# Kernel optimization log

Hardware: AMD Instinct MI355X
Metric: run time of the kernel (lower is better)

Reference implementation:

```python
import jax, jax.numpy as jnp
import numpy as np

K = 5              # kernel_size per pseudo dim
K3 = K ** 3        # 125 kernel weight slots
BITS = np.array([[(c >> d) & 1 for d in range(3)] for c in range(8)], dtype=np.int32)  # [8,3]
STRIDES = np.array([1, K, K * K], dtype=np.int32)

N0, E0 = 16384, 262144
N1, E1 = 4096, 65536
N2, E2 = 1024, 16384
N3, E3 = 256, 4096
B = 16
V = B * 8          # final dense 2x2x2 voxels per graph


def spline_conv(x, src, dst, pseudo, W, root, bias, num_nodes):
    """Degree-1 open B-spline conv (torch SplineConv, mean aggr + root + bias).
    x: [N,in], pseudo: [E,3] in [0,1], W: [K^3,in,out]."""
    v = pseudo * (K - 1)                         # [E,3]
    lo = jnp.clip(jnp.floor(v), 0, K - 2)
    frac = v - lo                                # [E,3]
    lo = lo.astype(jnp.int32)
    bits = jnp.asarray(BITS)                     # [8,3]
    idx = lo[:, None, :] + bits[None]            # [E,8,3]
    kidx = (idx * jnp.asarray(STRIDES)).sum(-1)  # [E,8] flat kernel index
    basis = jnp.where(bits[None].astype(bool), frac[:, None, :], 1.0 - frac[:, None, :]).prod(-1)  # [E,8]
    y = jnp.einsum('ni,kio->nko', x, W)          # [N,K3,out] per-node per-kernel transform
    yv = y[src[:, None], kidx]                   # [E,8,out] gather
    msg = (basis[..., None] * yv).sum(1)         # [E,out]
    agg = jax.ops.segment_sum(msg, dst, num_segments=num_nodes)
    deg = jax.ops.segment_sum(jnp.ones(dst.shape[0], x.dtype), dst, num_segments=num_nodes)
    agg = agg / jnp.maximum(deg, 1.0)[:, None]   # mean aggregation
    return agg + x @ root + bias


def pool_max(x, cluster, num_segments):
    p = jax.ops.segment_max(x, cluster, num_segments=num_segments)
    return jnp.where(jnp.isfinite(p), p, 0.0)    # empty voxels -> 0


def setup_inputs() -> dict:
    key = jax.random.key(0)
    ks = iter(jax.random.split(key, 64))
    f = lambda s, sc: jax.random.normal(next(ks), s, jnp.float32) * sc
    u = lambda s: jax.random.uniform(next(ks), s, jnp.float32)
    ri = lambda s, hi: jax.random.randint(next(ks), s, 0, hi, dtype=jnp.int32)
    return dict(
        x0=u((N0, 1)),
        pseudo0=u((E0, 3)), pseudo1=u((E1, 3)), pseudo2=u((E2, 3)), pseudo3=u((E3, 3)),
        W1=f((K3, 1, 32), 0.3), root1=f((1, 32), 0.3), b1=f((32,), 0.05),
        W2=f((K3, 32, 64), 0.05), root2=f((32, 64), 0.05), b2=f((64,), 0.05),
        W3=f((K3, 64, 64), 0.04), root3=f((64, 64), 0.04), b3=f((64,), 0.05),
        W4=f((K3, 64, 128), 0.04), root4=f((64, 128), 0.04), b4=f((128,), 0.05),
        fc1_w=f((1024, 256), 0.03), fc1_b=f((256,), 0.05),
        fc2_w=f((256, 10), 0.06), fc2_b=f((10,), 0.05),
        src0=ri((E0,), N0), dst0=ri((E0,), N0),
        src1=ri((E1,), N1), dst1=ri((E1,), N1),
        src2=ri((E2,), N2), dst2=ri((E2,), N2),
        src3=ri((E3,), N3), dst3=ri((E3,), N3),
        cluster0=ri((N0,), N1), cluster1=ri((N1,), N2),
        cluster2=ri((N2,), N3), cluster3=ri((N3,), V),
    )


def reference(x0, pseudo0, pseudo1, pseudo2, pseudo3,
              W1, root1, b1, W2, root2, b2, W3, root3, b3, W4, root4, b4,
              fc1_w, fc1_b, fc2_w, fc2_b,
              src0, dst0, src1, dst1, src2, dst2, src3, dst3,
              cluster0, cluster1, cluster2, cluster3):
    x = jax.nn.elu(spline_conv(x0, src0, dst0, pseudo0, W1, root1, b1, N0))
    x = pool_max(x, cluster0, N1)
    x = jax.nn.elu(spline_conv(x, src1, dst1, pseudo1, W2, root2, b2, N1))
    x = pool_max(x, cluster1, N2)
    x = jax.nn.elu(spline_conv(x, src2, dst2, pseudo2, W3, root3, b3, N2))
    x = pool_max(x, cluster2, N3)
    x = jax.nn.elu(spline_conv(x, src3, dst3, pseudo3, W4, root4, b4, N3))
    x = pool_max(x, cluster3, V)                 # [B*8, 128]
    x = x.reshape(B, 8 * 128)
    x = jax.nn.elu(x @ fc1_w + fc1_b)
    x = x @ fc2_w + fc2_b                        # dropout is a no-op in eval
    return jax.nn.log_softmax(x, axis=1)
```

## Files before the change

### kernel.cpp

```cpp
#include <hip/hip_runtime.h>
#include <hip/hip_bf16.h>
#include <math.h>

namespace {

constexpr int KK = 5;
constexpr int K3 = 125;
constexpr int N0 = 16384, E0 = 262144;
constexpr int N1 = 4096,  E1 = 65536;
constexpr int N2 = 1024,  E2 = 16384;
constexpr int N3 = 256,   E3 = 4096;
constexpr int NV = 128;
constexpr int BB = 16;

constexpr size_t OFF_AGG1 = 0;
constexpr size_t OFF_AGG2 = OFF_AGG1 + (size_t)N0 * 32;
constexpr size_t OFF_AGG3 = OFF_AGG2 + (size_t)N1 * 64;
constexpr size_t OFF_AGG4 = OFF_AGG3 + (size_t)N2 * 64;
constexpr size_t OFF_DEG1 = OFF_AGG4 + (size_t)N3 * 128;
constexpr size_t OFF_DEG2 = OFF_DEG1 + N0;
constexpr size_t OFF_DEG3 = OFF_DEG2 + N1;
constexpr size_t OFF_DEG4 = OFF_DEG3 + N2;
constexpr size_t ZERO_END = OFF_DEG4 + N3;

constexpr size_t OFF_PENC1 = ZERO_END;
constexpr size_t OFF_PENC2 = OFF_PENC1 + (size_t)N1 * 32;
constexpr size_t OFF_PENC3 = OFF_PENC2 + (size_t)N2 * 64;
constexpr size_t OFF_PENC4 = OFF_PENC3 + (size_t)N3 * 64;
constexpr size_t PENC_END  = OFF_PENC4 + (size_t)NV * 128;
constexpr size_t PENC_TOTAL = PENC_END - ZERO_END;

constexpr size_t OFF_X1 = PENC_END;
constexpr size_t OFF_P1 = OFF_X1 + (size_t)N0 * 32;
constexpr size_t OFF_X2 = OFF_P1 + (size_t)N1 * 32;
constexpr size_t OFF_P2 = OFF_X2 + (size_t)N1 * 64;
constexpr size_t OFF_X3 = OFF_P2 + (size_t)N2 * 64;
constexpr size_t OFF_P3 = OFF_X3 + (size_t)N2 * 64;
constexpr size_t OFF_X4 = OFF_P3 + (size_t)N3 * 64;
constexpr size_t OFF_P4 = OFF_X4 + (size_t)N3 * 128;
constexpr size_t OFF_FC1 = OFF_P4 + (size_t)NV * 128;
constexpr size_t WS_FLOATS = OFF_FC1 + (size_t)BB * 256;

constexpr size_t OFF_Y = WS_FLOATS;
constexpr size_t Y_ELEMS_MAX = (size_t)N1 * K3 * 64;
constexpr size_t WS_NEED_BYTES = OFF_Y * 4 + Y_ELEMS_MAX * 2;

__device__ __forceinline__ float eluf(float x) { return x > 0.f ? x : expm1f(x); }

__device__ __forceinline__ unsigned enc_f(float x) {
    unsigned u = __float_as_uint(x);
    return (u & 0x80000000u) ? ~u : (u | 0x80000000u);
}
__device__ __forceinline__ float dec_f(unsigned u) {
    u = (u & 0x80000000u) ? (u & 0x7fffffffu) : ~u;
    return __uint_as_float(u);
}

__device__ __forceinline__ void decode_edge(const float* __restrict__ pseudo, int e,
                                            float bas[8], int kid[8]) {
    float v0 = pseudo[e * 3 + 0] * (KK - 1);
    float v1 = pseudo[e * 3 + 1] * (KK - 1);
    float v2 = pseudo[e * 3 + 2] * (KK - 1);
    float f0 = fminf(fmaxf(floorf(v0), 0.f), (float)(KK - 2));
    float f1 = fminf(fmaxf(floorf(v1), 0.f), (float)(KK - 2));
    float f2 = fminf(fmaxf(floorf(v2), 0.f), (float)(KK - 2));
    int lo0 = (int)f0, lo1 = (int)f1, lo2 = (int)f2;
    float fr0 = v0 - f0, fr1 = v1 - f1, fr2 = v2 - f2;
#pragma unroll
    for (int c = 0; c < 8; ++c) {
        int b0 = c & 1, b1 = (c >> 1) & 1, b2 = (c >> 2) & 1;
        kid[c] = (lo0 + b0) + (lo1 + b1) * KK + (lo2 + b2) * KK * KK;
        bas[c] = (b0 ? fr0 : 1.f - fr0) * (b1 ? fr1 : 1.f - fr1) * (b2 ? fr2 : 1.f - fr2);
    }
}

__global__ void init_enc(unsigned* __restrict__ p, int n) {
    int g = blockIdx.x * blockDim.x + threadIdx.x;
    if (g < n) p[g] = 0x007FFFFFu;
}

__global__ void spline_l1(const float* __restrict__ x,
                          const float* __restrict__ pseudo,
                          const float* __restrict__ W1,
                          const int* __restrict__ src,
                          const int* __restrict__ dst,
                          float* __restrict__ agg,
                          float* __restrict__ deg, int E) {
    __shared__ float wlds[K3 * 32];
    int tid = threadIdx.x;
    for (int i = tid; i < K3 * 32; i += 256) wlds[i] = W1[i];
    __syncthreads();
    int o = tid & 31;
    int esub = tid >> 5;
    int ebase = blockIdx.x * 32 + esub;
#pragma unroll
    for (int r = 0; r < 4; ++r) {
        int e = ebase + r * 8;
        if (e >= E) continue;
        float bas[8]; int kid[8];
        decode_edge(pseudo, e, bas, kid);
        int s = src[e], dn = dst[e];
        float xv = x[s];
        float acc = 0.f;
#pragma unroll
        for (int c = 0; c < 8; ++c)
            acc = fmaf(bas[c], wlds[kid[c] * 32 + o], acc);
        atomicAdd(&agg[(size_t)dn * 32 + o], xv * acc);
        if (o == 0) atomicAdd(&deg[dn], 1.f);
    }
}

template <int IN, int OUT>
__global__ void gemm_y(const float* __restrict__ x,
                       const float* __restrict__ W,
                       __hip_bfloat16* __restrict__ y, int N) {
    constexpr int KO = K3 * OUT;
    __shared__ float xs[32][IN];
    int kt = blockIdx.x % (KO / 64);
    int n0 = (blockIdx.x / (KO / 64)) * 32;
    int tid = threadIdx.x;
    for (int idx = tid; idx < 32 * IN; idx += 256)
        xs[idx / IN][idx % IN] = x[(size_t)(n0 + idx / IN) * IN + idx % IN];
    __syncthreads();
    int col = kt * 64 + (tid & 63);
    int nsub = tid >> 6;
    int k = col / OUT, o = col % OUT;
    const float* Wp = W + (size_t)k * IN * OUT + o;
    float acc[8] = {0.f, 0.f, 0.f, 0.f, 0.f, 0.f, 0.f, 0.f};
#pragma unroll 4
    for (int i = 0; i < IN; ++i) {
        float w = Wp[(size_t)i * OUT];
#pragma unroll
        for (int j = 0; j < 8; ++j)
            acc[j] = fmaf(xs[nsub * 8 + j][i], w, acc[j]);
    }
#pragma unroll
    for (int j = 0; j < 8; ++j)
        y[(size_t)(n0 + nsub * 8 + j) * KO + col] = __float2bfloat16(acc[j]);
}

template <int OUT>
__global__ void gather_edge(const __hip_bfloat16* __restrict__ y,
                            const float* __restrict__ pseudo,
                            const int* __restrict__ src,
                            const int* __restrict__ dst,
                            float* __restrict__ agg,
                            float* __restrict__ deg, int E) {
    long long g = (long long)blockIdx.x * blockDim.x + threadIdx.x;
    int e = (int)(g / OUT);
    int o = (int)(g % OUT);
    if (e >= E) return;
    float bas[8]; int kid[8];
    decode_edge(pseudo, e, bas, kid);
    int s = src[e], dn = dst[e];
    const __hip_bfloat16* yp = y + (size_t)s * (K3 * OUT) + o;
    float acc = 0.f;
#pragma unroll
    for (int c = 0; c < 8; ++c)
        acc = fmaf(bas[c], __bfloat162float(yp[(size_t)kid[c] * OUT]), acc);
    atomicAdd(&agg[(size_t)dn * OUT + o], acc);
    if (o == 0) atomicAdd(&deg[dn], 1.f);
}

template <int IN, int OUT>
__global__ void spline_edge(const float* __restrict__ x,
                            const float* __restrict__ pseudo,
                            const float* __restrict__ W,
                            const int* __restrict__ src,
                            const int* __restrict__ dst,
                            float* __restrict__ agg,
                            float* __restrict__ deg, int E) {
    long long g = (long long)blockIdx.x * blockDim.x + threadIdx.x;
    int e = (int)(g / OUT);
    int o = (int)(g % OUT);
    if (e >= E) return;
    float bas[8]; int kid[8];
    decode_edge(pseudo, e, bas, kid);
    int s = src[e], dn = dst[e];
    const float* xp = x + (size_t)s * IN;
    float acc = 0.f;
#pragma unroll
    for (int c = 0; c < 8; ++c) {
        const float* Wp = W + (size_t)kid[c] * IN * OUT + o;
        float sacc = 0.f;
        for (int i = 0; i < IN; ++i)
            sacc = fmaf(xp[i], Wp[(size_t)i * OUT], sacc);
        acc = fmaf(bas[c], sacc, acc);
    }
    atomicAdd(&agg[(size_t)dn * OUT + o], acc);
    if (o == 0) atomicAdd(&deg[dn], 1.f);
}

template <int IN, int OUT>
__global__ void node_finish(const float* __restrict__ agg,
                            const float* __restrict__ deg,
                            const float* __restrict__ x,
                            const float* __restrict__ root,
                            const float* __restrict__ bias,
                            float* __restrict__ out, int N) {
    int g = blockIdx.x * blockDim.x + threadIdx.x;
    if (g >= N * OUT) return;
    int n = g / OUT, o = g % OUT;
    float r = 0.f;
    for (int i = 0; i < IN; ++i)
        r = fmaf(x[(size_t)n * IN + i], root[(size_t)i * OUT + o], r);
    float dg = fmaxf(deg[n], 1.f);
    float val = agg[g] / dg + r + bias[o];
    out[g] = eluf(val);
}

template <int C>
__global__ void pool_scatter(const float* __restrict__ x,
                             const int* __restrict__ cluster,
                             unsigned* __restrict__ penc, int N) {
    int g = blockIdx.x * blockDim.x + threadIdx.x;
    if (g >= N * C) return;
    int n = g / C, c = g % C;
    atomicMax(&penc[(size_t)cluster[n] * C + c], enc_f(x[g]));
}

__global__ void pool_final(const unsigned* __restrict__ penc,
                           float* __restrict__ out, int M) {
    int g = blockIdx.x * blockDim.x + threadIdx.x;
    if (g >= M) return;
    float v = dec_f(penc[g]);
    out[g] = isfinite(v) ? v : 0.f;
}

__global__ void fc1_kernel(const float* __restrict__ xin,
                           const float* __restrict__ w,
                           const float* __restrict__ b,
                           float* __restrict__ out) {
    int bq = blockIdx.x;
    int p = threadIdx.x;
    const float* xr = xin + (size_t)bq * 1024;
    float acc = b[p];
    for (int q = 0; q < 1024; ++q)
        acc = fmaf(xr[q], w[(size_t)q * 256 + p], acc);
    out[(size_t)bq * 256 + p] = eluf(acc);
}

__global__ void fc2_ls_kernel(const float* __restrict__ xin,
                              const float* __restrict__ w,
                              const float* __restrict__ b,
                              float* __restrict__ out) {
    __shared__ float l[10];
    __shared__ float red[2];
    int bq = blockIdx.x;
    int t = threadIdx.x;
    if (t < 10) {
        const float* xr = xin + (size_t)bq * 256;
        float acc = b[t];
        for (int q = 0; q < 256; ++q)
            acc = fmaf(xr[q], w[(size_t)q * 10 + t], acc);
        l[t] = acc;
    }
    __syncthreads();
    if (t == 0) {
        float m = l[0];
        for (int i = 1; i < 10; ++i) m = fmaxf(m, l[i]);
        float s = 0.f;
        for (int i = 0; i < 10; ++i) s += expf(l[i] - m);
        red[0] = m;
        red[1] = logf(s);
    }
    __syncthreads();
    if (t < 10) out[(size_t)bq * 10 + t] = l[t] - red[0] - red[1];
}

inline unsigned blk(long long t) { return (unsigned)((t + 255) / 256); }

}

extern "C" void kernel_launch(void* const* d_in, const int* in_sizes, int n_in,
                              void* d_out, int out_size, void* d_ws, size_t ws_size,
                              hipStream_t stream) {
    const float* x0    = (const float*)d_in[0];
    const float* ps0   = (const float*)d_in[1];
    const float* ps1   = (const float*)d_in[2];
    const float* ps2   = (const float*)d_in[3];
    const float* ps3   = (const float*)d_in[4];
    const float* W1    = (const float*)d_in[5];
    const float* root1 = (const float*)d_in[6];
    const float* b1    = (const float*)d_in[7];
    const float* W2    = (const float*)d_in[8];
    const float* root2 = (const float*)d_in[9];
    const float* b2    = (const float*)d_in[10];
    const float* W3    = (const float*)d_in[11];
    const float* root3 = (const float*)d_in[12];
    const float* b3    = (const float*)d_in[13];
    const float* W4    = (const float*)d_in[14];
    const float* root4 = (const float*)d_in[15];
    const float* b4    = (const float*)d_in[16];
    const float* fc1w  = (const float*)d_in[17];
    const float* fc1b  = (const float*)d_in[18];
    const float* fc2w  = (const float*)d_in[19];
    const float* fc2b  = (const float*)d_in[20];
    const int* src0 = (const int*)d_in[21];
    const int* dst0 = (const int*)d_in[22];
    const int* src1 = (const int*)d_in[23];
    const int* dst1 = (const int*)d_in[24];
    const int* src2 = (const int*)d_in[25];
    const int* dst2 = (const int*)d_in[26];
    const int* src3 = (const int*)d_in[27];
    const int* dst3 = (const int*)d_in[28];
    const int* cl0  = (const int*)d_in[29];
    const int* cl1  = (const int*)d_in[30];
    const int* cl2  = (const int*)d_in[31];
    const int* cl3  = (const int*)d_in[32];

    float* ws = (float*)d_ws;
    float* out = (float*)d_out;
    __hip_bfloat16* yb = (__hip_bfloat16*)(ws + OFF_Y);
    const bool use_y = (ws_size >= WS_NEED_BYTES);

    hipMemsetAsync(ws + OFF_AGG1, 0, ZERO_END * sizeof(float), stream);
    init_enc<<<blk(PENC_TOTAL), 256, 0, stream>>>((unsigned*)(ws + OFF_PENC1), (int)PENC_TOTAL);

    spline_l1<<<E0 / 32, 256, 0, stream>>>(x0, ps0, W1, src0, dst0,
                                           ws + OFF_AGG1, ws + OFF_DEG1, E0);
    node_finish<1, 32><<<blk((long long)N0 * 32), 256, 0, stream>>>(
        ws + OFF_AGG1, ws + OFF_DEG1, x0, root1, b1, ws + OFF_X1, N0);
    pool_scatter<32><<<blk((long long)N0 * 32), 256, 0, stream>>>(
        ws + OFF_X1, cl0, (unsigned*)(ws + OFF_PENC1), N0);
    pool_final<<<blk((long long)N1 * 32), 256, 0, stream>>>(
        (unsigned*)(ws + OFF_PENC1), ws + OFF_P1, N1 * 32);

    if (use_y) {
        gemm_y<32, 64><<<(N1 / 32) * (K3 * 64 / 64), 256, 0, stream>>>(ws + OFF_P1, W2, yb, N1);
        gather_edge<64><<<blk((long long)E1 * 64), 256, 0, stream>>>(
            yb, ps1, src1, dst1, ws + OFF_AGG2, ws + OFF_DEG2, E1);
    } else {
        spline_edge<32, 64><<<blk((long long)E1 * 64), 256, 0, stream>>>(
            ws + OFF_P1, ps1, W2, src1, dst1, ws + OFF_AGG2, ws + OFF_DEG2, E1);
    }
    node_finish<32, 64><<<blk((long long)N1 * 64), 256, 0, stream>>>(
        ws + OFF_AGG2, ws + OFF_DEG2, ws + OFF_P1, root2, b2, ws + OFF_X2, N1);
    pool_scatter<64><<<blk((long long)N1 * 64), 256, 0, stream>>>(
        ws + OFF_X2, cl1, (unsigned*)(ws + OFF_PENC2), N1);
    pool_final<<<blk((long long)N2 * 64), 256, 0, stream>>>(
        (unsigned*)(ws + OFF_PENC2), ws + OFF_P2, N2 * 64);

    if (use_y) {
        gemm_y<64, 64><<<(N2 / 32) * (K3 * 64 / 64), 256, 0, stream>>>(ws + OFF_P2, W3, yb, N2);
        gather_edge<64><<<blk((long long)E2 * 64), 256, 0, stream>>>(
            yb, ps2, src2, dst2, ws + OFF_AGG3, ws + OFF_DEG3, E2);
    } else {
        spline_edge<64, 64><<<blk((long long)E2 * 64), 256, 0, stream>>>(
            ws + OFF_P2, ps2, W3, src2, dst2, ws + OFF_AGG3, ws + OFF_DEG3, E2);
    }
    node_finish<64, 64><<<blk((long long)N2 * 64), 256, 0, stream>>>(
        ws + OFF_AGG3, ws + OFF_DEG3, ws + OFF_P2, root3, b3, ws + OFF_X3, N2);
    pool_scatter<64><<<blk((long long)N2 * 64), 256, 0, stream>>>(
        ws + OFF_X3, cl2, (unsigned*)(ws + OFF_PENC3), N2);
    pool_final<<<blk((long long)N3 * 64), 256, 0, stream>>>(
        (unsigned*)(ws + OFF_PENC3), ws + OFF_P3, N3 * 64);

    if (use_y) {
        gemm_y<64, 128><<<(N3 / 32) * (K3 * 128 / 64), 256, 0, stream>>>(ws + OFF_P3, W4, yb, N3);
        gather_edge<128><<<blk((long long)E3 * 128), 256, 0, stream>>>(
            yb, ps3, src3, dst3, ws + OFF_AGG4, ws + OFF_DEG4, E3);
    } else {
        spline_edge<64, 128><<<blk((long long)E3 * 128), 256, 0, stream>>>(
            ws + OFF_P3, ps3, W4, src3, dst3, ws + OFF_AGG4, ws + OFF_DEG4, E3);
    }
    node_finish<64, 128><<<blk((long long)N3 * 128), 256, 0, stream>>>(
        ws + OFF_AGG4, ws + OFF_DEG4, ws + OFF_P3, root4, b4, ws + OFF_X4, N3);
    pool_scatter<128><<<blk((long long)N3 * 128), 256, 0, stream>>>(
        ws + OFF_X4, cl3, (unsigned*)(ws + OFF_PENC4), N3);
    pool_final<<<blk((long long)NV * 128), 256, 0, stream>>>(
        (unsigned*)(ws + OFF_PENC4), ws + OFF_P4, NV * 128);

    fc1_kernel<<<16, 256, 0, stream>>>(ws + OFF_P4, fc1w, fc1b, ws + OFF_FC1);
    fc2_ls_kernel<<<16, 64, 0, stream>>>(ws + OFF_FC1, fc2w, fc2b, out);
}
```

Before: 380.7 us.

## Use bf16 MFMA for per-node kernel transform and precompute edge basis tables

New measurement: 371.4 us. 2.4% less time.

```diff
diff --git a/kernel.cpp b/kernel.cpp
--- a/kernel.cpp
+++ b/kernel.cpp
@@ -3,6 +3,10 @@
 #include <math.h>
 
 namespace {
+
+typedef unsigned long long u64;
+typedef __attribute__((ext_vector_type(8))) short bf16x8;
+typedef __attribute__((ext_vector_type(4))) float f32x4;
 
 constexpr int KK = 5;
 constexpr int K3 = 125;
@@ -41,9 +45,17 @@
 constexpr size_t OFF_FC1 = OFF_P4 + (size_t)NV * 128;
 constexpr size_t WS_FLOATS = OFF_FC1 + (size_t)BB * 256;
 
-constexpr size_t OFF_Y = WS_FLOATS;
-constexpr size_t Y_ELEMS_MAX = (size_t)N1 * K3 * 64;
-constexpr size_t WS_NEED_BYTES = OFF_Y * 4 + Y_ELEMS_MAX * 2;
+constexpr size_t OFF_BAS = WS_FLOATS;
+constexpr size_t OFF_KID = OFF_BAS + (size_t)E0 * 8;
+constexpr size_t TAB_END = OFF_KID + (size_t)E0 * 2;
+constexpr size_t OFF_XB  = TAB_END;
+constexpr size_t OFF_WT  = OFF_XB + (size_t)N1 * 32 / 2;
+constexpr size_t OFF_Y   = OFF_WT + (size_t)16000 * 64 / 2;
+constexpr size_t Y_FLOATS = (size_t)N1 * K3 * 64 / 2;
+constexpr size_t WS_END  = OFF_Y + Y_FLOATS;
+
+constexpr size_t WS_NEED_TAB = TAB_END * sizeof(float);
+constexpr size_t WS_NEED_Y   = WS_END * sizeof(float);
 
 __device__ __forceinline__ float eluf(float x) { return x > 0.f ? x : expm1f(x); }
 
@@ -54,6 +66,13 @@
 __device__ __forceinline__ float dec_f(unsigned u) {
     u = (u & 0x80000000u) ? (u & 0x7fffffffu) : ~u;
     return __uint_as_float(u);
+}
+__device__ __forceinline__ float bf2f(unsigned short u) {
+    return __uint_as_float((unsigned)u << 16);
+}
+__device__ __forceinline__ unsigned short f2bf(float v) {
+    __hip_bfloat16 h = __float2bfloat16(v);
+    return *reinterpret_cast<unsigned short*>(&h);
 }
 
 __device__ __forceinline__ void decode_edge(const float* __restrict__ pseudo, int e,
@@ -77,6 +96,57 @@
 __global__ void init_enc(unsigned* __restrict__ p, int n) {
     int g = blockIdx.x * blockDim.x + threadIdx.x;
     if (g < n) p[g] = 0x007FFFFFu;
+}
+
+__global__ void decode_basis(const float* __restrict__ pseudo,
+                             float* __restrict__ bas, u64* __restrict__ kid, int E) {
+    int e = blockIdx.x * blockDim.x + threadIdx.x;
+    if (e >= E) return;
+    float b[8]; int k[8];
+    decode_edge(pseudo, e, b, k);
+    float4 q0 = make_float4(b[0], b[1], b[2], b[3]);
+    float4 q1 = make_float4(b[4], b[5], b[6], b[7]);
+    *(float4*)(bas + (size_t)e * 8) = q0;
+    *(float4*)(bas + (size_t)e * 8 + 4) = q1;
+    u64 p = 0;
+#pragma unroll
+    for (int c = 0; c < 8; ++c) p |= (u64)(unsigned)k[c] << (8 * c);
+    kid[e] = p;
+}
+
+__global__ void spline_l1_t(const float* __restrict__ x,
+                            const float* __restrict__ bas,
+                            const u64* __restrict__ kid,
+                            const float* __restrict__ W1,
+                            const int* __restrict__ src,
+                            const int* __restrict__ dst,
+                            float* __restrict__ agg,
+                            float* __restrict__ deg, int E) {
+    __shared__ float wlds[K3 * 32];
+    int tid = threadIdx.x;
+    for (int i = tid; i < K3 * 32; i += 256) wlds[i] = W1[i];
+    __syncthreads();
+    int o = tid & 31;
+    int esub = tid >> 5;
+#pragma unroll
+    for (int r = 0; r < 8; ++r) {
+        int e = blockIdx.x * 64 + r * 8 + esub;
+        if (e >= E) continue;
+        float4 q0 = *(const float4*)(bas + (size_t)e * 8);
+        float4 q1 = *(const float4*)(bas + (size_t)e * 8 + 4);
+        float b[8] = {q0.x, q0.y, q0.z, q0.w, q1.x, q1.y, q1.z, q1.w};
+        u64 k8 = kid[e];
+        int s = src[e], dn = dst[e];
+        float xv = x[s];
+        float acc = 0.f;
+#pragma unroll
+        for (int c = 0; c < 8; ++c) {
+            int kc = (int)((k8 >> (8 * c)) & 255u);
+            acc = fmaf(b[c], wlds[kc * 32 + o], acc);
+        }
+        atomicAdd(&agg[(size_t)dn * 32 + o], xv * acc);
+        if (o == 0) atomicAdd(&deg[dn], 1.f);
+    }
 }
 
 __global__ void spline_l1(const float* __restrict__ x,
@@ -92,72 +162,100 @@
     __syncthreads();
     int o = tid & 31;
     int esub = tid >> 5;
-    int ebase = blockIdx.x * 32 + esub;
 #pragma unroll
     for (int r = 0; r < 4; ++r) {
-        int e = ebase + r * 8;
+        int e = blockIdx.x * 32 + r * 8 + esub;
         if (e >= E) continue;
-        float bas[8]; int kid[8];
-        decode_edge(pseudo, e, bas, kid);
+        float bas[8]; int kidv[8];
+        decode_edge(pseudo, e, bas, kidv);
         int s = src[e], dn = dst[e];
         float xv = x[s];
         float acc = 0.f;
 #pragma unroll
         for (int c = 0; c < 8; ++c)
-            acc = fmaf(bas[c], wlds[kid[c] * 32 + o], acc);
+            acc = fmaf(bas[c], wlds[kidv[c] * 32 + o], acc);
         atomicAdd(&agg[(size_t)dn * 32 + o], xv * acc);
         if (o == 0) atomicAdd(&deg[dn], 1.f);
     }
 }
 
+__global__ void conv_x(const float* __restrict__ in, unsigned short* __restrict__ out, int n) {
+    int g = blockIdx.x * blockDim.x + threadIdx.x;
+    if (g < n) out[g] = f2bf(in[g]);
+}
+
 template <int IN, int OUT>
-__global__ void gemm_y(const float* __restrict__ x,
-                       const float* __restrict__ W,
-                       __hip_bfloat16* __restrict__ y, int N) {
-    constexpr int KO = K3 * OUT;
-    __shared__ float xs[32][IN];
-    int kt = blockIdx.x % (KO / 64);
-    int n0 = (blockIdx.x / (KO / 64)) * 32;
-    int tid = threadIdx.x;
-    for (int idx = tid; idx < 32 * IN; idx += 256)
-        xs[idx / IN][idx % IN] = x[(size_t)(n0 + idx / IN) * IN + idx % IN];
-    __syncthreads();
-    int col = kt * 64 + (tid & 63);
-    int nsub = tid >> 6;
-    int k = col / OUT, o = col % OUT;
-    const float* Wp = W + (size_t)k * IN * OUT + o;
-    float acc[8] = {0.f, 0.f, 0.f, 0.f, 0.f, 0.f, 0.f, 0.f};
-#pragma unroll 4
-    for (int i = 0; i < IN; ++i) {
-        float w = Wp[(size_t)i * OUT];
-#pragma unroll
-        for (int j = 0; j < 8; ++j)
-            acc[j] = fmaf(xs[nsub * 8 + j][i], w, acc[j]);
-    }
-#pragma unroll
-    for (int j = 0; j < 8; ++j)
-        y[(size_t)(n0 + nsub * 8 + j) * KO + col] = __float2bfloat16(acc[j]);
+__global__ void conv_w(const float* __restrict__ W, unsigned short* __restrict__ wt, int total) {
+    int g = blockIdx.x * blockDim.x + threadIdx.x;
+    if (g >= total) return;
+    int i = g % IN;
+    int ko = g / IN;
+    int k = ko / OUT, o = ko % OUT;
+    wt[g] = f2bf(W[(size_t)k * IN * OUT + (size_t)i * OUT + o]);
+}
+
+template <int IN>
+__global__ __launch_bounds__(256) void gemm_y_mfma(const unsigned short* __restrict__ xb,
+                                                   const unsigned short* __restrict__ wt,
+                                                   unsigned short* __restrict__ y,
+                                                   int N, int KO) {
+    int wid = (blockIdx.x * 256 + threadIdx.x) >> 6;
+    int lane = threadIdx.x & 63;
+    int nTiles = N >> 4;
+    int n0 = (wid % nTiles) << 4;
+    int ko0 = (wid / nTiles) << 6;
+    int l15 = lane & 15;
+    int kk = (lane >> 4) << 3;
+
+    f32x4 acc[4];
+#pragma unroll
+    for (int t = 0; t < 4; ++t) acc[t] = (f32x4){0.f, 0.f, 0.f, 0.f};
+
+#pragma unroll
+    for (int s = 0; s < IN / 32; ++s) {
+        bf16x8 bfrag = *(const bf16x8*)(xb + (size_t)(n0 + l15) * IN + s * 32 + kk);
+#pragma unroll
+        for (int t = 0; t < 4; ++t) {
+            bf16x8 afrag = *(const bf16x8*)(wt + (size_t)(ko0 + t * 16 + l15) * IN + s * 32 + kk);
+            acc[t] = __builtin_amdgcn_mfma_f32_16x16x32_bf16(afrag, bfrag, acc[t], 0, 0, 0);
+        }
+    }
+    int rbase = (lane >> 4) << 2;
+#pragma unroll
+    for (int t = 0; t < 4; ++t) {
+        ushort4 sv;
+        sv.x = f2bf(acc[t][0]);
+        sv.y = f2bf(acc[t][1]);
+        sv.z = f2bf(acc[t][2]);
+        sv.w = f2bf(acc[t][3]);
+        *(ushort4*)(y + (size_t)(n0 + l15) * KO + ko0 + t * 16 + rbase) = sv;
+    }
 }
 
 template <int OUT>
-__global__ void gather_edge(const __hip_bfloat16* __restrict__ y,
-                            const float* __restrict__ pseudo,
-                            const int* __restrict__ src,
-                            const int* __restrict__ dst,
-                            float* __restrict__ agg,
-                            float* __restrict__ deg, int E) {
-    long long g = (long long)blockIdx.x * blockDim.x + threadIdx.x;
-    int e = (int)(g / OUT);
-    int o = (int)(g % OUT);
+__global__ void gather_edge_t(const unsigned short* __restrict__ y,
+                              const float* __restrict__ bas,
+                              const u64* __restrict__ kid,
+                              const int* __restrict__ src,
+                              const int* __restrict__ dst,
+                              float* __restrict__ agg,
+                              float* __restrict__ deg, int E) {
+    int g = blockIdx.x * blockDim.x + threadIdx.x;
+    int e = g / OUT;
+    int o = g % OUT;
     if (e >= E) return;
-    float bas[8]; int kid[8];
-    decode_edge(pseudo, e, bas, kid);
+    float4 q0 = *(const float4*)(bas + (size_t)e * 8);
+    float4 q1 = *(const float4*)(bas + (size_t)e * 8 + 4);
+    float b[8] = {q0.x, q0.y, q0.z, q0.w, q1.x, q1.y, q1.z, q1.w};
+    u64 k8 = kid[e];
     int s = src[e], dn = dst[e];
-    const __hip_bfloat16* yp = y + (size_t)s * (K3 * OUT) + o;
+    const unsigned short* yp = y + (size_t)s * (K3 * OUT) + o;
     float acc = 0.f;
 #pragma unroll
-    for (int c = 0; c < 8; ++c)
-        acc = fmaf(bas[c], __bfloat162float(yp[(size_t)kid[c] * OUT]), acc);
+    for (int c = 0; c < 8; ++c) {
+        int kc = (int)((k8 >> (8 * c)) & 255u);
+        acc = fmaf(b[c], bf2f(yp[(size_t)kc * OUT]), acc);
+    }
     atomicAdd(&agg[(size_t)dn * OUT + o], acc);
     if (o == 0) atomicAdd(&deg[dn], 1.f);
 }
@@ -174,14 +272,14 @@
     int e = (int)(g / OUT);
     int o = (int)(g % OUT);
     if (e >= E) return;
-    float bas[8]; int kid[8];
-    decode_edge(pseudo, e, bas, kid);
+    float bas[8]; int kidv[8];
+    decode_edge(pseudo, e, bas, kidv);
     int s = src[e], dn = dst[e];
     const float* xp = x + (size_t)s * IN;
     float acc = 0.f;
 #pragma unroll
     for (int c = 0; c < 8; ++c) {
-        const float* Wp = W + (size_t)kid[c] * IN * OUT + o;
+        const float* Wp = W + (size_t)kidv[c] * IN * OUT + o;
         float sacc = 0.f;
         for (int i = 0; i < IN; ++i)
             sacc = fmaf(xp[i], Wp[(size_t)i * OUT], sacc);
@@ -311,14 +409,25 @@
 
     float* ws = (float*)d_ws;
     float* out = (float*)d_out;
-    __hip_bfloat16* yb = (__hip_bfloat16*)(ws + OFF_Y);
-    const bool use_y = (ws_size >= WS_NEED_BYTES);
+    float* bas = ws + OFF_BAS;
+    u64*   kid = (u64*)(ws + OFF_KID);
+    unsigned short* xb = (unsigned short*)(ws + OFF_XB);
+    unsigned short* wt = (unsigned short*)(ws + OFF_WT);
+    unsigned short* yb = (unsigned short*)(ws + OFF_Y);
+    const bool use_tab = (ws_size >= WS_NEED_TAB);
+    const bool use_y   = (ws_size >= WS_NEED_Y);
 
     hipMemsetAsync(ws + OFF_AGG1, 0, ZERO_END * sizeof(float), stream);
     init_enc<<<blk(PENC_TOTAL), 256, 0, stream>>>((unsigned*)(ws + OFF_PENC1), (int)PENC_TOTAL);
 
-    spline_l1<<<E0 / 32, 256, 0, stream>>>(x0, ps0, W1, src0, dst0,
-                                           ws + OFF_AGG1, ws + OFF_DEG1, E0);
+    if (use_tab) {
+        decode_basis<<<blk(E0), 256, 0, stream>>>(ps0, bas, kid, E0);
+        spline_l1_t<<<E0 / 64, 256, 0, stream>>>(x0, bas, kid, W1, src0, dst0,
+                                                 ws + OFF_AGG1, ws + OFF_DEG1, E0);
+    } else {
+        spline_l1<<<E0 / 32, 256, 0, stream>>>(x0, ps0, W1, src0, dst0,
+                                               ws + OFF_AGG1, ws + OFF_DEG1, E0);
+    }
     node_finish<1, 32><<<blk((long long)N0 * 32), 256, 0, stream>>>(
         ws + OFF_AGG1, ws + OFF_DEG1, x0, root1, b1, ws + OFF_X1, N0);
     pool_scatter<32><<<blk((long long)N0 * 32), 256, 0, stream>>>(
@@ -327,9 +436,12 @@
         (unsigned*)(ws + OFF_PENC1), ws + OFF_P1, N1 * 32);
 
     if (use_y) {
-        gemm_y<32, 64><<<(N1 / 32) * (K3 * 64 / 64), 256, 0, stream>>>(ws + OFF_P1, W2, yb, N1);
-        gather_edge<64><<<blk((long long)E1 * 64), 256, 0, stream>>>(
-            yb, ps1, src1, dst1, ws + OFF_AGG2, ws + OFF_DEG2, E1);
+        conv_x<<<blk((long long)N1 * 32), 256, 0, stream>>>(ws + OFF_P1, xb, N1 * 32);
+        conv_w<32, 64><<<blk((long long)K3 * 64 * 32), 256, 0, stream>>>(W2, wt, K3 * 64 * 32);
+        gemm_y_mfma<32><<<(N1 / 16) * (K3 * 64 / 64) / 4, 256, 0, stream>>>(xb, wt, yb, N1, K3 * 64);
+        decode_basis<<<blk(E1), 256, 0, stream>>>(ps1, bas, kid, E1);
+        gather_edge_t<64><<<blk((long long)E1 * 64), 256, 0, stream>>>(
+            yb, bas, kid, src1, dst1, ws + OFF_AGG2, ws + OFF_DEG2, E1);
     } else {
         spline_edge<32, 64><<<blk((long long)E1 * 64), 256, 0, stream>>>(
             ws + OFF_P1, ps1, W2, src1, dst1, ws + OFF_AGG2, ws + OFF_DEG2, E1);
@@ -342,9 +454,12 @@
         (unsigned*)(ws + OFF_PENC2), ws + OFF_P2, N2 * 64);
 
     if (use_y) {
-        gemm_y<64, 64><<<(N2 / 32) * (K3 * 64 / 64), 256, 0, stream>>>(ws + OFF_P2, W3, yb, N2);
-        gather_edge<64><<<blk((long long)E2 * 64), 256, 0, stream>>>(
-            yb, ps2, src2, dst2, ws + OFF_AGG3, ws + OFF_DEG3, E2);
+        conv_x<<<blk((long long)N2 * 64), 256, 0, stream>>>(ws + OFF_P2, xb, N2 * 64);
+        conv_w<64, 64><<<blk((long long)K3 * 64 * 64), 256, 0, stream>>>(W3, wt, K3 * 64 * 64);
+        gemm_y_mfma<64><<<(N2 / 16) * (K3 * 64 / 64) / 4, 256, 0, stream>>>(xb, wt, yb, N2, K3 * 64);
+        decode_basis<<<blk(E2), 256, 0, stream>>>(ps2, bas, kid, E2);
+        gather_edge_t<64><<<blk((long long)E2 * 64), 256, 0, stream>>>(
+            yb, bas, kid, src2, dst2, ws + OFF_AGG3, ws + OFF_DEG3, E2);
     } else {
         spline_edge<64, 64><<<blk((long long)E2 * 64), 256, 0, stream>>>(
             ws + OFF_P2, ps2, W3, src2, dst2, ws + OFF_AGG3, ws + OFF_DEG3, E2);
@@ -357,9 +472,12 @@
         (unsigned*)(ws + OFF_PENC3), ws + OFF_P3, N3 * 64);
 
     if (use_y) {
-        gemm_y<64, 128><<<(N3 / 32) * (K3 * 128 / 64), 256, 0, stream>>>(ws + OFF_P3, W4, yb, N3);
-        gather_edge<128><<<blk((long long)E3 * 128), 256, 0, stream>>>(
-            yb, ps3, src3, dst3, ws + OFF_AGG4, ws + OFF_DEG4, E3);
+        conv_x<<<blk((long long)N3 * 64), 256, 0, stream>>>(ws + OFF_P3, xb, N3 * 64);
+        conv_w<64, 128><<<blk((long long)K3 * 128 * 64), 256, 0, stream>>>(W4, wt, K3 * 128 * 64);
+        gemm_y_mfma<64><<<(N3 / 16) * (K3 * 128 / 64) / 4, 256, 0, stream>>>(xb, wt, yb, N3, K3 * 128);
+        decode_basis<<<blk(E3), 256, 0, stream>>>(ps3, bas, kid, E3);
+        gather_edge_t<128><<<blk((long long)E3 * 128), 256, 0, stream>>>(
+            yb, bas, kid, src3, dst3, ws + OFF_AGG4, ws + OFF_DEG4, E3);
     } else {
         spline_edge<64, 128><<<blk((long long)E3 * 128), 256, 0, stream>>>(
             ws + OFF_P3, ps3, W4, src3, dst3, ws + OFF_AGG4, ws + OFF_DEG4, E3);
```
